# Performance work log

Hardware: AMD Instinct MI355X
Metric: run time of the kernel (lower is better)

The kernel has to match this reference:

```python
import jax, jax.numpy as jnp
import numpy as np

B, T, E, H = 2, 2048, 1024, 16
D = E // H


def setup_inputs() -> dict:
    key = jax.random.key(0)
    ks = jax.random.split(key, 8)
    k = jax.random.normal(ks[0], (B, T, E), dtype=jnp.float32)
    q = jax.random.normal(ks[1], (B, T, E), dtype=jnp.float32)
    v = jax.random.normal(ks[2], (B, T, E), dtype=jnp.float32)
    # torch Linear weights: [out, in]; y = x @ W.T (+ b)
    Wk = jax.random.normal(ks[3], (E, E), dtype=jnp.float32) * 0.02
    Wq = jax.random.normal(ks[4], (E, E), dtype=jnp.float32) * 0.02
    Wv = jax.random.normal(ks[5], (E, E), dtype=jnp.float32) * 0.02
    Wo = jax.random.normal(ks[6], (E, E), dtype=jnp.float32) * 0.02
    bo = jax.random.normal(ks[7], (E,), dtype=jnp.float32) * 0.02
    # causal mask: True = masked (as in masked_fill)
    mask = jnp.triu(jnp.ones((T, T), dtype=bool), k=1)
    return {"k": k, "q": q, "v": v, "Wk": Wk, "Wq": Wq, "Wv": Wv,
            "Wo": Wo, "bo": bo, "mask": mask}


def _split_heads(x):  # [b,t,(h d)] -> [b,h,t,d]
    b, t, _ = x.shape
    return x.reshape(b, t, H, D).transpose(0, 2, 1, 3)


def reference(k, q, v, Wk, Wq, Wv, Wo, bo, mask):
    keys = _split_heads(k @ Wk.T)      # no bias (add_bias_kv=False)
    queries = _split_heads(q @ Wq.T)   # q_prj has bias=False always
    values = _split_heads(v @ Wv.T)
    # scores [b,h,t,t]; original applies mask (-inf) then divides by sqrt(d)
    att = jnp.einsum('bhqd,bhkd->bhqk', queries, keys)
    att = jnp.where(mask, -jnp.inf, att)
    att = jax.nn.softmax(att / jnp.sqrt(jnp.float32(D)), axis=-1)
    out = jnp.einsum('bhqk,bhkd->bhqd', att, values)
    out = out.transpose(0, 2, 1, 3).reshape(B, T, E)  # merge heads
    return out @ Wo.T + bo
```

## Files before the change

kernel.cpp:

```cpp
#include <hip/hip_runtime.h>
#include <stdint.h>

typedef __bf16 bf16;
typedef bf16 bf16x8 __attribute__((ext_vector_type(8)));
typedef bf16 bf16x4 __attribute__((ext_vector_type(4)));
typedef float f32x4 __attribute__((ext_vector_type(4)));
typedef float f32x16 __attribute__((ext_vector_type(16)));
typedef unsigned int uint;
typedef uint u32x4 __attribute__((ext_vector_type(4)));

#define MFMA16(a, b, c) __builtin_amdgcn_mfma_f32_16x16x32_bf16(a, b, c, 0, 0, 0)
#define MFMA32(a, b, c) __builtin_amdgcn_mfma_f32_32x32x16_bf16(a, b, c, 0, 0, 0)

static constexpr int Bsz = 2, T = 2048, E = 1024, H = 16, Dh = 64;
static constexpr float QSCALE = 0.125f * 1.44269504088896f;

__device__ __forceinline__ float exp2fast(float x) {
#if __has_builtin(__builtin_amdgcn_exp2f)
    return __builtin_amdgcn_exp2f(x);
#else
    return exp2f(x);
#endif
}

__device__ __forceinline__ void gll16(const bf16* g, bf16* l) {
    __builtin_amdgcn_global_load_lds((const __attribute__((address_space(1))) uint*)g,
                                     (__attribute__((address_space(3))) uint*)l, 16, 0, 0);
}

template <int ROWS>
__device__ __forceinline__ void stage_b16(bf16* lds, const bf16* g, int ldg, int wave, int lane) {
#pragma unroll
    for (int i = 0; i < ROWS / 32; ++i) {
        const int row = wave * (ROWS / 4) + i * 8;
        gll16(g + (size_t)(row + (lane >> 3)) * ldg + (lane & 7) * 8, lds + row * 64);
    }
}
template <int ROWS>
__device__ __forceinline__ void stage_f32(bf16* lds, const float* g, int ldg, int tid) {
#pragma unroll
    for (int i = 0; i < ROWS / 16; ++i) {
        int gg = tid + i * 256;
        int row = gg >> 4, c4 = (gg & 15) << 2;
        const float4 v = *(const float4*)(g + (size_t)row * ldg + c4);
        bf16x4 bv = {(bf16)v.x, (bf16)v.y, (bf16)v.z, (bf16)v.w};
        *(bf16x4*)(lds + row * 64 + c4) = bv;
    }
}

template <bool AB16, bool BB16, int MF, int NF, bool OUTF32>
__device__ __forceinline__ void gemm_body(bf16* At, bf16* Bt,
                                          const bf16* A16, const float* A32,
                                          const bf16* B16, const float* B32,
                                          bf16* Yb, float* Yf, const float* bias,
                                          int m0, int n0, int K, int ldy, float oscale) {
    constexpr int BM = MF * 32, BN = NF * 32;
    const int tid = threadIdx.x, lane = tid & 63, wave = tid >> 6;
    const int wm = wave >> 1, wn = wave & 1;
    const int fr = lane & 15, kg = (lane >> 4) << 3;

    f32x4 acc[MF][NF] = {};

    for (int k0 = 0; k0 < K; k0 += 64) {
        if constexpr (AB16)
            stage_b16<BM>(At, A16 + (size_t)m0 * K + k0, K, wave, lane);
        else
            stage_f32<BM>(At, A32 + (size_t)m0 * K + k0, K, tid);
        if constexpr (BB16)
            stage_b16<BN>(Bt, B16 + (size_t)n0 * K + k0, K, wave, lane);
        else
            stage_f32<BN>(Bt, B32 + (size_t)n0 * K + k0, K, tid);
        __syncthreads();
#pragma unroll
        for (int kk = 0; kk < 64; kk += 32) {
            bf16x8 af[MF], bfr[NF];
#pragma unroll
            for (int f = 0; f < MF; ++f)
                af[f] = *(const bf16x8*)(At + (wm * (BM / 2) + f * 16 + fr) * 64 + kk + kg);
#pragma unroll
            for (int f = 0; f < NF; ++f)
                bfr[f] = *(const bf16x8*)(Bt + (wn * (BN / 2) + f * 16 + fr) * 64 + kk + kg);
#pragma unroll
            for (int mf = 0; mf < MF; ++mf)
#pragma unroll
                for (int nf = 0; nf < NF; ++nf)
                    acc[mf][nf] = MFMA16(af[mf], bfr[nf], acc[mf][nf]);
        }
        __syncthreads();
    }
    const int rb = (lane >> 4) << 2;
#pragma unroll
    for (int mf = 0; mf < MF; ++mf)
#pragma unroll
        for (int nf = 0; nf < NF; ++nf) {
            int n = n0 + wn * (BN / 2) + nf * 16 + fr;
            float bn = 0.f;
            if constexpr (OUTF32) bn = bias[n];
#pragma unroll
            for (int r = 0; r < 4; ++r) {
                int mm = m0 + wm * (BM / 2) + mf * 16 + rb + r;
                float v = acc[mf][nf][r];
                if constexpr (OUTF32)
                    Yf[(size_t)mm * ldy + n] = v + bn;
                else
                    Yb[(size_t)mm * ldy + n] = (bf16)(v * oscale);
            }
        }
}

__global__ __launch_bounds__(256) void cvt_w(const float* Wq, const float* Wk,
                                             const float* Wv, const float* Wo,
                                             bf16* Wqc, bf16* Wkc, bf16* Wvc, bf16* Woc) {
    const size_t NW = (size_t)E * E;
    const size_t nwork = (4 * NW) >> 2;
    for (size_t t = (size_t)blockIdx.x * 256 + threadIdx.x; t < nwork;
         t += (size_t)gridDim.x * 256) {
        size_t i = t << 2;
        size_t w = i / NW;
        size_t off = i - w * NW;
        const float* s = w == 0 ? Wq : (w == 1 ? Wk : (w == 2 ? Wv : Wo));
        bf16* d = w == 0 ? Wqc : (w == 1 ? Wkc : (w == 2 ? Wvc : Woc));
        const float4 x = *(const float4*)(s + off);
        bf16x4 y = {(bf16)x.x, (bf16)x.y, (bf16)x.z, (bf16)x.w};
        *(bf16x4*)(d + off) = y;
    }
}

template <bool XB16, bool WB16>
__global__ __launch_bounds__(256) void qkv_proj(
    const float* q32, const float* k32, const float* v32,
    const bf16* q16, const bf16* k16, const bf16* v16,
    const float* Wq32, const float* Wk32, const float* Wv32,
    const bf16* Wq16, const bf16* Wk16, const bf16* Wv16,
    bf16* Qb, bf16* Kb, bf16* Vt) {
    __shared__ bf16 At[128 * 64];
    __shared__ bf16 Bt[128 * 64];
    const int bid = blockIdx.x;
    const int wid = (bid & 7) * 96 + (bid >> 3);
    if (wid < 512) {
        int s = wid >> 8;
        int t = wid & 255;
        int m0 = (t >> 3) * 128, n0 = (t & 7) * 128;
        gemm_body<XB16, WB16, 4, 4, false>(At, Bt,
                                           s ? k16 : q16, s ? k32 : q32,
                                           s ? Wk16 : Wq16, s ? Wk32 : Wq32,
                                           s ? Kb : Qb, nullptr, nullptr, m0, n0, E, E,
                                           s ? 1.0f : QSCALE);
    } else {
        int r = wid - 512;
        int b = r >> 7, rr = r & 127;
        int m0 = (rr >> 4) * 128, n0 = (rr & 15) * 128;
        gemm_body<WB16, XB16, 4, 4, false>(At, Bt,
                                           Wv16, Wv32,
                                           v16 + (size_t)b * T * E, v32 + (size_t)b * T * E,
                                           Vt + (size_t)b * E * T, nullptr, nullptr,
                                           m0, n0, E, T, 1.0f);
    }
}

template <bool WB16>
__global__ __launch_bounds__(256) void out_proj(const bf16* Xb, const bf16* W16,
                                                const float* W32, float* Y,
                                                const float* bias) {
    __shared__ bf16 At[64 * 64];
    __shared__ bf16 Bt[128 * 64];
    const int bid = blockIdx.x;
    const int wid = (bid & 7) * 64 + (bid >> 3);
    const int m0 = (wid >> 3) * 64, n0 = (wid & 7) * 128;
    gemm_body<true, WB16, 2, 4, true>(At, Bt, Xb, nullptr, W16, W32, nullptr, Y, bias,
                                      m0, n0, E, E, 1.0f);
}

__device__ __forceinline__ uint pkbf(float a, float b) {
    uint16_t x = __builtin_bit_cast(uint16_t, (bf16)a);
    uint16_t y = __builtin_bit_cast(uint16_t, (bf16)b);
    return (uint)x | ((uint)y << 16);
}

template <int DMODE>
__device__ __forceinline__ void attn_tile64(const bf16* KL, const bf16* VL,
                                            int l31, int hi, int swz,
                                            const bf16x8 (&qf)[4],
                                            f32x16& o0, f32x16& o1, float& m, float& l) {
    constexpr int NCC = (DMODE == 2) ? 2 : 4;
    f32x16 s0 = {}, s1 = {};
    {
        bf16x8 kf[4];
#pragma unroll
        for (int t = 0; t < 4; ++t)
            kf[t] = *(const bf16x8*)(KL + l31 * 64 + ((((t << 1) | hi) ^ swz) << 3));
        __builtin_amdgcn_s_setprio(1);
#pragma unroll
        for (int t = 0; t < 4; ++t) s0 = MFMA32(kf[t], qf[t], s0);
        __builtin_amdgcn_s_setprio(0);
    }
    if constexpr (DMODE != 2) {
        bf16x8 kf[4];
#pragma unroll
        for (int t = 0; t < 4; ++t)
            kf[t] = *(const bf16x8*)(KL + (32 + l31) * 64 + ((((t << 1) | hi) ^ swz) << 3));
        __builtin_amdgcn_s_setprio(1);
#pragma unroll
        for (int t = 0; t < 4; ++t) s1 = MFMA32(kf[t], qf[t], s1);
        __builtin_amdgcn_s_setprio(0);
    }
    bf16x8 vfa[NCC], vfb[NCC];
#pragma unroll
    for (int cc = 0; cc < NCC; ++cc) {
        vfa[cc] = *(const bf16x8*)(VL + l31 * 64 + ((((cc << 1) | hi) ^ swz) << 3));
        vfb[cc] = *(const bf16x8*)(VL + (32 + l31) * 64 + ((((cc << 1) | hi) ^ swz) << 3));
    }
    if constexpr (DMODE == 2) {
#pragma unroll
        for (int r = 0; r < 16; ++r) {
            int key = (r & 3) + 8 * (r >> 2) + 4 * hi;
            if (key > l31) s0[r] = -1e30f;
        }
    }
    if constexpr (DMODE == 1) {
#pragma unroll
        for (int r = 0; r < 16; ++r) {
            int key = (r & 3) + 8 * (r >> 2) + 4 * hi;
            if (key > l31) s1[r] = -1e30f;
        }
    }
    float t8[8];
    if constexpr (DMODE == 2) {
#pragma unroll
        for (int r = 0; r < 8; ++r) t8[r] = fmaxf(s0[r], s0[r + 8]);
    } else {
#pragma unroll
        for (int r = 0; r < 8; ++r)
            t8[r] = fmaxf(fmaxf(s0[r], s0[r + 8]), fmaxf(s1[r], s1[r + 8]));
    }
#pragma unroll
    for (int r = 0; r < 4; ++r) t8[r] = fmaxf(t8[r], t8[r + 4]);
    float pm = fmaxf(fmaxf(t8[0], t8[1]), fmaxf(t8[2], t8[3]));
    pm = fmaxf(pm, __shfl_xor(pm, 32, 64));

    if (!__all(pm - m <= 11.5f)) {
        float mn = fmaxf(m, pm);
        float al = exp2fast(m - mn);
        m = mn;
        l *= al;
#pragma unroll
        for (int r = 0; r < 16; ++r) {
            int qr = (r & 3) + 8 * (r >> 2) + 4 * hi;
            float aq = __shfl(al, qr, 64);
            o0[r] *= aq;
            o1[r] *= aq;
        }
    }
#pragma unroll
    for (int r = 0; r < 16; ++r) s0[r] = exp2fast(s0[r] - m);
    if constexpr (DMODE != 2) {
#pragma unroll
        for (int r = 0; r < 16; ++r) s1[r] = exp2fast(s1[r] - m);
    }
    float u8[8];
    if constexpr (DMODE == 2) {
#pragma unroll
        for (int r = 0; r < 8; ++r) u8[r] = s0[r] + s0[r + 8];
    } else {
#pragma unroll
        for (int r = 0; r < 8; ++r) u8[r] = (s0[r] + s0[r + 8]) + (s1[r] + s1[r + 8]);
    }
#pragma unroll
    for (int r = 0; r < 4; ++r) u8[r] = u8[r] + u8[r + 4];
    float ps = (u8[0] + u8[1]) + (u8[2] + u8[3]);
    l += ps + __shfl_xor(ps, 32, 64);

    __builtin_amdgcn_s_setprio(1);
#pragma unroll
    for (int cc = 0; cc < NCC; ++cc) {
        const f32x16& ph = (cc < 2) ? s0 : s1;
        const int bse = (cc & 1) * 8;
        uint x0 = pkbf(ph[bse + 0], ph[bse + 1]);
        uint x1 = pkbf(ph[bse + 2], ph[bse + 3]);
        uint y0 = pkbf(ph[bse + 4], ph[bse + 5]);
        uint y1 = pkbf(ph[bse + 6], ph[bse + 7]);
        uint sx0 = __shfl_xor(x0, 32, 64), sx1 = __shfl_xor(x1, 32, 64);
        uint sy0 = __shfl_xor(y0, 32, 64), sy1 = __shfl_xor(y1, 32, 64);
        u32x4 wv;
        wv.x = hi ? sy0 : x0;
        wv.y = hi ? sy1 : x1;
        wv.z = hi ? y0 : sx0;
        wv.w = hi ? y1 : sx1;
        bf16x8 pa = __builtin_bit_cast(bf16x8, wv);
        o0 = MFMA32(pa, vfa[cc], o0);
        o1 = MFMA32(pa, vfb[cc], o1);
    }
    __builtin_amdgcn_s_setprio(0);
}

__global__ __launch_bounds__(256) void attn_fwd(const bf16* __restrict__ Q,
                                                const bf16* __restrict__ K,
                                                const bf16* __restrict__ Vt,
                                                bf16* __restrict__ O) {
    __shared__ __align__(16) bf16 Kl[2][64 * 64];
    __shared__ __align__(16) bf16 Vl[2][64 * 64];

    const int g = blockIdx.x;
    const int lo = g & 255;
    const int xcd = lo & 7, jj = lo >> 3;
    const int hb = xcd * 4 + (jj & 3);
    const int qhi = 15 - (jj >> 2);
    const int qb = (g < 256) ? qhi : 15 - qhi;
    const int h = hb & 15, b = hb >> 4;

    const int tid = threadIdx.x, lane = tid & 63, w = tid >> 6;
    const int l31 = lane & 31, hi = lane >> 5;
    const int q0 = qb * 128 + w * 32;

    const bf16* Qp = Q + (size_t)b * T * E + h * Dh;
    const bf16* Kp = K + (size_t)b * T * E + h * Dh;
    const bf16* Vp = Vt + ((size_t)b * E + h * Dh) * T;

    const int rsub = lane >> 3;
    const int csw = (lane & 7) ^ rsub;
    const int swz = (l31 & 7);

    bf16x8 qf[4];
#pragma unroll
    for (int t = 0; t < 4; ++t)
        qf[t] = *(const bf16x8*)(Qp + (size_t)(q0 + l31) * E + t * 16 + hi * 8);

    f32x16 o0 = {}, o1 = {};
    float m = -1e30f, l = 0.f;
    const int ktD = 2 * qb + (w >> 1);
    const int nK2 = 2 * qb + 2;

#pragma unroll
    for (int ii = 0; ii < 2; ++ii)
        gll16(Kp + (size_t)(16 * w + 8 * ii + rsub) * E + csw * 8, &Kl[0][(2 * w + ii) * 512]);
#pragma unroll
    for (int ii = 0; ii < 2; ++ii)
        gll16(Vp + (size_t)(16 * w + 8 * ii + rsub) * T + csw * 8, &Vl[0][(2 * w + ii) * 512]);

    int cur = 0;
#pragma unroll 1
    for (int K2 = 0; K2 < nK2; ++K2) {
        if (K2 + 1 < nK2) {
            const int kb = (K2 + 1) * 64;
            const bf16* Kg = Kp + (size_t)kb * E;
            const bf16* Vg = Vp + kb;
            bf16* dK = &Kl[cur ^ 1][0];
            bf16* dV = &Vl[cur ^ 1][0];
#pragma unroll
            for (int ii = 0; ii < 2; ++ii)
                gll16(Kg + (size_t)(16 * w + 8 * ii + rsub) * E + csw * 8, dK + (2 * w + ii) * 512);
#pragma unroll
            for (int ii = 0; ii < 2; ++ii)
                gll16(Vg + (size_t)(16 * w + 8 * ii + rsub) * T + csw * 8, dV + (2 * w + ii) * 512);
            asm volatile("s_waitcnt vmcnt(4)" ::: "memory");
        } else {
            asm volatile("s_waitcnt vmcnt(0)" ::: "memory");
        }
        __builtin_amdgcn_s_barrier();
        asm volatile("" ::: "memory");

        const bf16* KL = &Kl[cur][0];
        const bf16* VL = &Vl[cur][0];
        if (K2 < ktD) {
            attn_tile64<0>(KL, VL, l31, hi, swz, qf, o0, o1, m, l);
        } else if (K2 == ktD) {
            if (w & 1)
                attn_tile64<1>(KL, VL, l31, hi, swz, qf, o0, o1, m, l);
            else
                attn_tile64<2>(KL, VL, l31, hi, swz, qf, o0, o1, m, l);
        }
        asm volatile("" ::: "memory");
        __builtin_amdgcn_s_barrier();
        cur ^= 1;
    }

    bf16* Op = O + (size_t)b * T * E + h * Dh;
#pragma unroll
    for (int r = 0; r < 16; ++r) {
        int qr = (r & 3) + 8 * (r >> 2) + 4 * hi;
        float lq = __shfl(l, qr, 64);
        float inv = 1.0f / lq;
        Op[(size_t)(q0 + qr) * E + l31] = (bf16)(o0[r] * inv);
        Op[(size_t)(q0 + qr) * E + 32 + l31] = (bf16)(o1[r] * inv);
    }
}

extern "C" void kernel_launch(void* const* d_in, const int* in_sizes, int n_in,
                              void* d_out, int out_size, void* d_ws, size_t ws_size,
                              hipStream_t stream) {
    const float* k_in = (const float*)d_in[0];
    const float* q_in = (const float*)d_in[1];
    const float* v_in = (const float*)d_in[2];
    const float* Wk = (const float*)d_in[3];
    const float* Wq = (const float*)d_in[4];
    const float* Wv = (const float*)d_in[5];
    const float* Wo = (const float*)d_in[6];
    const float* bo = (const float*)d_in[7];
    float* out = (float*)d_out;

    const size_t NE = (size_t)Bsz * T * E;
    const size_t NW = (size_t)E * E;
    bf16* ws = (bf16*)d_ws;
    bf16* Qb = ws;
    bf16* Kb = ws + NE;
    bf16* Vt = ws + 2 * NE;
    bf16* Ab = ws + 3 * NE;
    bf16* Wqc = ws + 4 * NE;
    bf16* Wkc = Wqc + NW;
    bf16* Wvc = Wkc + NW;
    bf16* Woc = Wvc + NW;

    const bool planB = ws_size >= (4 * NE + 4 * NW) * sizeof(bf16);

    if (planB) {
        cvt_w<<<512, 256, 0, stream>>>(Wq, Wk, Wv, Wo, Wqc, Wkc, Wvc, Woc);
        qkv_proj<false, true><<<768, 256, 0, stream>>>(
            q_in, k_in, v_in, nullptr, nullptr, nullptr,
            nullptr, nullptr, nullptr, Wqc, Wkc, Wvc, Qb, Kb, Vt);
    } else {
        qkv_proj<false, false><<<768, 256, 0, stream>>>(
            q_in, k_in, v_in, nullptr, nullptr, nullptr,
            Wq, Wk, Wv, nullptr, nullptr, nullptr, Qb, Kb, Vt);
    }

    attn_fwd<<<dim3(512), 256, 0, stream>>>(Qb, Kb, Vt, Ab);

    if (planB)
        out_proj<true><<<512, 256, 0, stream>>>(Ab, Woc, nullptr, out, bo);
    else
        out_proj<false><<<512, 256, 0, stream>>>(Ab, nullptr, Wo, out, bo);
}
```

Baseline: 144.0 us.

## Stage fp32 GEMM operands to LDS via direct loads and swizzle tiles

Result: faster. 129.5 us (-10.1%).

```diff
diff --git a/kernel.cpp b/kernel.cpp
--- a/kernel.cpp
+++ b/kernel.cpp
@@ -30,56 +30,82 @@
 
 template <int ROWS>
 __device__ __forceinline__ void stage_b16(bf16* lds, const bf16* g, int ldg, int wave, int lane) {
+    const int rsub = lane >> 3;
+    const int csw = (lane & 7) ^ rsub;
 #pragma unroll
     for (int i = 0; i < ROWS / 32; ++i) {
         const int row = wave * (ROWS / 4) + i * 8;
-        gll16(g + (size_t)(row + (lane >> 3)) * ldg + (lane & 7) * 8, lds + row * 64);
-    }
-}
+        gll16(g + (size_t)(row + rsub) * ldg + csw * 8, lds + row * 64);
+    }
+}
+__device__ __forceinline__ bf16x8 frag_b16(const bf16* lds, int r, int cc) {
+    return *(const bf16x8*)(lds + r * 64 + ((cc ^ (r & 7)) << 3));
+}
+
 template <int ROWS>
-__device__ __forceinline__ void stage_f32(bf16* lds, const float* g, int ldg, int tid) {
+__device__ __forceinline__ void stage_f32lds(float* lds, const float* g, int ldg,
+                                             int wave, int lane) {
+    const int rsub = lane >> 4;
 #pragma unroll
     for (int i = 0; i < ROWS / 16; ++i) {
-        int gg = tid + i * 256;
-        int row = gg >> 4, c4 = (gg & 15) << 2;
-        const float4 v = *(const float4*)(g + (size_t)row * ldg + c4);
-        bf16x4 bv = {(bf16)v.x, (bf16)v.y, (bf16)v.z, (bf16)v.w};
-        *(bf16x4*)(lds + row * 64 + c4) = bv;
-    }
-}
-
-template <bool AB16, bool BB16, int MF, int NF, bool OUTF32>
-__device__ __forceinline__ void gemm_body(bf16* At, bf16* Bt,
-                                          const bf16* A16, const float* A32,
-                                          const bf16* B16, const float* B32,
+        const int slab = wave * (ROWS / 16) + i;
+        const int row0 = slab * 4;
+        const int src = (lane & 15) ^ ((((slab & 3)) << 2) | rsub);
+        gll16((const bf16*)(g + (size_t)(row0 + rsub) * ldg + src * 4),
+              (bf16*)(lds + row0 * 64));
+    }
+}
+__device__ __forceinline__ bf16x8 frag_f32(const float* lds, int r, int lc0) {
+    const f32x4 u0 = *(const f32x4*)(lds + r * 64 + ((lc0 ^ (r & 15)) << 2));
+    const f32x4 u1 = *(const f32x4*)(lds + r * 64 + (((lc0 + 1) ^ (r & 15)) << 2));
+    bf16x8 a = {(bf16)u0.x, (bf16)u0.y, (bf16)u0.z, (bf16)u0.w,
+                (bf16)u1.x, (bf16)u1.y, (bf16)u1.z, (bf16)u1.w};
+    return a;
+}
+
+template <bool AF32, bool BF32, int MF, int NF, bool OUTF32>
+__device__ __forceinline__ void gemm_body(char* smem, const void* Ap, const void* Bp,
                                           bf16* Yb, float* Yf, const float* bias,
                                           int m0, int n0, int K, int ldy, float oscale) {
     constexpr int BM = MF * 32, BN = NF * 32;
+    constexpr int ASZ = BM * 64 * (AF32 ? 4 : 2);
     const int tid = threadIdx.x, lane = tid & 63, wave = tid >> 6;
     const int wm = wave >> 1, wn = wave & 1;
-    const int fr = lane & 15, kg = (lane >> 4) << 3;
+    const int fr = lane & 15, kg16 = lane >> 4;
 
     f32x4 acc[MF][NF] = {};
 
     for (int k0 = 0; k0 < K; k0 += 64) {
-        if constexpr (AB16)
-            stage_b16<BM>(At, A16 + (size_t)m0 * K + k0, K, wave, lane);
+        if constexpr (AF32)
+            stage_f32lds<BM>((float*)smem, (const float*)Ap + (size_t)m0 * K + k0, K, wave, lane);
         else
-            stage_f32<BM>(At, A32 + (size_t)m0 * K + k0, K, tid);
-        if constexpr (BB16)
-            stage_b16<BN>(Bt, B16 + (size_t)n0 * K + k0, K, wave, lane);
+            stage_b16<BM>((bf16*)smem, (const bf16*)Ap + (size_t)m0 * K + k0, K, wave, lane);
+        if constexpr (BF32)
+            stage_f32lds<BN>((float*)(smem + ASZ), (const float*)Bp + (size_t)n0 * K + k0,
+                             K, wave, lane);
         else
-            stage_f32<BN>(Bt, B32 + (size_t)n0 * K + k0, K, tid);
+            stage_b16<BN>((bf16*)(smem + ASZ), (const bf16*)Bp + (size_t)n0 * K + k0,
+                          K, wave, lane);
         __syncthreads();
 #pragma unroll
         for (int kk = 0; kk < 64; kk += 32) {
             bf16x8 af[MF], bfr[NF];
 #pragma unroll
-            for (int f = 0; f < MF; ++f)
-                af[f] = *(const bf16x8*)(At + (wm * (BM / 2) + f * 16 + fr) * 64 + kk + kg);
-#pragma unroll
-            for (int f = 0; f < NF; ++f)
-                bfr[f] = *(const bf16x8*)(Bt + (wn * (BN / 2) + f * 16 + fr) * 64 + kk + kg);
+            for (int f = 0; f < MF; ++f) {
+                const int r = wm * (BM / 2) + f * 16 + fr;
+                if constexpr (AF32)
+                    af[f] = frag_f32((const float*)smem, r, (kk >> 2) + (kg16 << 1));
+                else
+                    af[f] = frag_b16((const bf16*)smem, r, (kk >> 3) + kg16);
+            }
+#pragma unroll
+            for (int f = 0; f < NF; ++f) {
+                const int r = wn * (BN / 2) + f * 16 + fr;
+                if constexpr (BF32)
+                    bfr[f] = frag_f32((const float*)(smem + ASZ), r, (kk >> 2) + (kg16 << 1));
+                else
+                    bfr[f] = frag_b16((const bf16*)(smem + ASZ), r, (kk >> 3) + kg16);
+            }
 #pragma unroll
             for (int mf = 0; mf < MF; ++mf)
 #pragma unroll
@@ -126,49 +152,54 @@
     }
 }
 
-template <bool XB16, bool WB16>
+template <bool PB>
 __global__ __launch_bounds__(256) void qkv_proj(
     const float* q32, const float* k32, const float* v32,
-    const bf16* q16, const bf16* k16, const bf16* v16,
+    const bf16* Wq16, const bf16* Wk16, const bf16* Wv16,
     const float* Wq32, const float* Wk32, const float* Wv32,
-    const bf16* Wq16, const bf16* Wk16, const bf16* Wv16,
     bf16* Qb, bf16* Kb, bf16* Vt) {
-    __shared__ bf16 At[128 * 64];
-    __shared__ bf16 Bt[128 * 64];
+    __shared__ __align__(16) char smem[PB ? 48 * 1024 : 64 * 1024];
     const int bid = blockIdx.x;
     const int wid = (bid & 7) * 96 + (bid >> 3);
     if (wid < 512) {
         int s = wid >> 8;
         int t = wid & 255;
         int m0 = (t >> 3) * 128, n0 = (t & 7) * 128;
-        gemm_body<XB16, WB16, 4, 4, false>(At, Bt,
-                                           s ? k16 : q16, s ? k32 : q32,
-                                           s ? Wk16 : Wq16, s ? Wk32 : Wq32,
-                                           s ? Kb : Qb, nullptr, nullptr, m0, n0, E, E,
-                                           s ? 1.0f : QSCALE);
+        if constexpr (PB)
+            gemm_body<true, false, 4, 4, false>(smem, s ? k32 : q32, s ? Wk16 : Wq16,
+                                                s ? Kb : Qb, nullptr, nullptr, m0, n0, E, E,
+                                                s ? 1.0f : QSCALE);
+        else
+            gemm_body<true, true, 4, 4, false>(smem, s ? k32 : q32, s ? Wk32 : Wq32,
+                                               s ? Kb : Qb, nullptr, nullptr, m0, n0, E, E,
+                                               s ? 1.0f : QSCALE);
     } else {
         int r = wid - 512;
         int b = r >> 7, rr = r & 127;
         int m0 = (rr >> 4) * 128, n0 = (rr & 15) * 128;
-        gemm_body<WB16, XB16, 4, 4, false>(At, Bt,
-                                           Wv16, Wv32,
-                                           v16 + (size_t)b * T * E, v32 + (size_t)b * T * E,
-                                           Vt + (size_t)b * E * T, nullptr, nullptr,
-                                           m0, n0, E, T, 1.0f);
-    }
-}
-
-template <bool WB16>
+        if constexpr (PB)
+            gemm_body<false, true, 4, 4, false>(smem, Wv16, v32 + (size_t)b * T * E,
+                                                Vt + (size_t)b * E * T, nullptr, nullptr,
+                                                m0, n0, E, T, 1.0f);
+        else
+            gemm_body<true, true, 4, 4, false>(smem, Wv32, v32 + (size_t)b * T * E,
+                                               Vt + (size_t)b * E * T, nullptr, nullptr,
+                                               m0, n0, E, T, 1.0f);
+    }
+}
+
+template <bool PB>
 __global__ __launch_bounds__(256) void out_proj(const bf16* Xb, const bf16* W16,
                                                 const float* W32, float* Y,
                                                 const float* bias) {
-    __shared__ bf16 At[64 * 64];
-    __shared__ bf16 Bt[128 * 64];
+    __shared__ __align__(16) char smem[PB ? 24 * 1024 : 40 * 1024];
     const int bid = blockIdx.x;
     const int wid = (bid & 7) * 64 + (bid >> 3);
     const int m0 = (wid >> 3) * 64, n0 = (wid & 7) * 128;
-    gemm_body<true, WB16, 2, 4, true>(At, Bt, Xb, nullptr, W16, W32, nullptr, Y, bias,
-                                      m0, n0, E, E, 1.0f);
+    if constexpr (PB)
+        gemm_body<false, false, 2, 4, true>(smem, Xb, W16, nullptr, Y, bias, m0, n0, E, E, 1.0f);
+    else
+        gemm_body<false, true, 2, 4, true>(smem, Xb, W32, nullptr, Y, bias, m0, n0, E, E, 1.0f);
 }
 
 __device__ __forceinline__ uint pkbf(float a, float b) {
@@ -414,13 +445,11 @@
 
     if (planB) {
         cvt_w<<<512, 256, 0, stream>>>(Wq, Wk, Wv, Wo, Wqc, Wkc, Wvc, Woc);
-        qkv_proj<false, true><<<768, 256, 0, stream>>>(
-            q_in, k_in, v_in, nullptr, nullptr, nullptr,
-            nullptr, nullptr, nullptr, Wqc, Wkc, Wvc, Qb, Kb, Vt);
+        qkv_proj<true><<<768, 256, 0, stream>>>(q_in, k_in, v_in, Wqc, Wkc, Wvc,
+                                                nullptr, nullptr, nullptr, Qb, Kb, Vt);
     } else {
-        qkv_proj<false, false><<<768, 256, 0, stream>>>(
-            q_in, k_in, v_in, nullptr, nullptr, nullptr,
-            Wq, Wk, Wv, nullptr, nullptr, nullptr, Qb, Kb, Vt);
+        qkv_proj<false><<<768, 256, 0, stream>>>(q_in, k_in, v_in, nullptr, nullptr, nullptr,
+                                                 Wq, Wk, Wv, Qb, Kb, Vt);
     }
 
     attn_fwd<<<dim3(512), 256, 0, stream>>>(Qb, Kb, Vt, Ab);
```
